# Kernel tuning notes

Hardware: AMD Instinct MI355X
Metric: run time of the kernel (lower is better)

Reference implementation:

```python
import jax, jax.numpy as jnp
import numpy as np

B, C, H, W = 4, 256, 64, 64
G = 32          # GroupNorm groups
EPS = 1e-6


def setup_inputs() -> dict:
    key = jax.random.key(0)
    ks = jax.random.split(key, 6)
    inp = {
        "x": jax.random.normal(ks[0], (B, C, H, W), dtype=jnp.float32),
        "gamma": jnp.ones((C,), jnp.float32),
        "beta": jnp.zeros((C,), jnp.float32),
        "wq": jax.random.normal(ks[1], (C, C), jnp.float32) * 0.02,
        "bq": jnp.zeros((C,), jnp.float32),
        "wk": jax.random.normal(ks[2], (C, C), jnp.float32) * 0.02,
        "bk": jnp.zeros((C,), jnp.float32),
        "wv": jax.random.normal(ks[3], (C, C), jnp.float32) * 0.02,
        "bv": jnp.zeros((C,), jnp.float32),
        "wp": jax.random.normal(ks[4], (C, C), jnp.float32) * 0.02,
        "bp": jnp.zeros((C,), jnp.float32),
    }
    return inp


def _group_norm(x, gamma, beta):
    b, c, h, w = x.shape
    xs = x.reshape(b, G, c // G, h, w)
    mu = xs.mean(axis=(2, 3, 4), keepdims=True)
    var = xs.var(axis=(2, 3, 4), keepdims=True)  # biased, matches torch GroupNorm
    xn = ((xs - mu) * jax.lax.rsqrt(var + EPS)).reshape(b, c, h, w)
    return xn * gamma[None, :, None, None] + beta[None, :, None, None]


def _conv1x1(s, w, bias):
    # 1x1 conv == per-pixel channel matmul
    return jnp.einsum('oc,bchw->bohw', w, s) + bias[None, :, None, None]


def reference(x, gamma, beta, wq, bq, wk, bk, wv, bv, wp, bp):
    b, c, h, w = x.shape
    s = _group_norm(x, gamma, beta)
    q = _conv1x1(s, wq, bq).reshape(b, c, h * w)  # [B, C, N]
    k = _conv1x1(s, wk, bk).reshape(b, c, h * w)
    v = _conv1x1(s, wv, bv).reshape(b, c, h * w)
    # scores[b,i,j] = sum_c q[b,c,i] k[b,c,j], scaled by C^-1/2
    scores = jnp.einsum('bci,bcj->bij', q, k) * (c ** -0.5)
    attn = jax.nn.softmax(scores, axis=2)
    # h_[b,c,i] = sum_j v[b,c,j] attn[b,i,j]
    h_ = jnp.einsum('bij,bcj->bci', attn, v).reshape(b, c, h, w)
    h_ = _conv1x1(h_, wp, bp)
    return x + h_
```

## Files before the change

### kernel.cpp

```cpp
#include <hip/hip_runtime.h>

#define BB 4
#define CCH 256
#define NPIX 4096
#define EPS 1e-6f

typedef __attribute__((ext_vector_type(8))) short bf16x8;
typedef __attribute__((ext_vector_type(4))) float f32x4;

__device__ __forceinline__ unsigned short f2bf(float f) {
    return (unsigned short)((__float_as_uint(f) + 0x8000u) >> 16);
}
__device__ __forceinline__ float bf2f(unsigned short h) {
    return __uint_as_float((unsigned)h << 16);
}
__device__ __forceinline__ void gl2lds16(const void* g, void* l) {
    __builtin_amdgcn_global_load_lds(
        (const __attribute__((address_space(1))) unsigned int*)g,
        (__attribute__((address_space(3))) unsigned int*)l, 16, 0, 0);
}

__global__ __launch_bounds__(256) void gn_apply(const float* __restrict__ x,
                                                const float* __restrict__ gamma,
                                                const float* __restrict__ beta,
                                                unsigned short* __restrict__ sb) {
    int bg = blockIdx.x;
    int b = bg >> 5, g = bg & 31;
    const float4* x4 = (const float4*)(x + (size_t)(b * CCH + g * 8) * NPIX);
    float s = 0.f, ss = 0.f;
    for (int e = threadIdx.x; e < 8 * NPIX / 4; e += 256) {
        float4 v = x4[e];
        s += v.x + v.y + v.z + v.w;
        ss += v.x * v.x + v.y * v.y + v.z * v.z + v.w * v.w;
    }
    __shared__ float rs[256], rss[256];
    __shared__ float mean_s, rstd_s;
    rs[threadIdx.x] = s; rss[threadIdx.x] = ss;
    __syncthreads();
    for (int off = 128; off > 0; off >>= 1) {
        if (threadIdx.x < (unsigned)off) {
            rs[threadIdx.x] += rs[threadIdx.x + off];
            rss[threadIdx.x] += rss[threadIdx.x + off];
        }
        __syncthreads();
    }
    if (threadIdx.x == 0) {
        const float inv = 1.0f / (float)(8 * NPIX);
        float m = rs[0] * inv;
        float var = rss[0] * inv - m * m;
        mean_s = m;
        rstd_s = rsqrtf(var + EPS);
    }
    __syncthreads();
    float scale[8], shift[8];
#pragma unroll
    for (int ci = 0; ci < 8; ++ci) {
        float ga = gamma[g * 8 + ci], be = beta[g * 8 + ci];
        scale[ci] = rstd_s * ga;
        shift[ci] = be - mean_s * scale[ci];
    }
#pragma unroll 1
    for (int r = 0; r < 4; ++r) {
        int pq = r * 256 + threadIdx.x;
        __align__(16) unsigned short h[4][8];
#pragma unroll
        for (int ci = 0; ci < 8; ++ci) {
            float4 v = x4[ci * 1024 + pq];
            h[0][ci] = f2bf(v.x * scale[ci] + shift[ci]);
            h[1][ci] = f2bf(v.y * scale[ci] + shift[ci]);
            h[2][ci] = f2bf(v.z * scale[ci] + shift[ci]);
            h[3][ci] = f2bf(v.w * scale[ci] + shift[ci]);
        }
        size_t base = ((size_t)(b * NPIX + pq * 4) << 8) + g * 8;
#pragma unroll
        for (int p = 0; p < 4; ++p)
            *(uint4*)(sb + base + (size_t)p * 256) = *(const uint4*)h[p];
    }
}

__global__ __launch_bounds__(256) void wcvt(const float* __restrict__ wq,
                                            const float* __restrict__ wk,
                                            const float* __restrict__ wv,
                                            const float* __restrict__ wp,
                                            unsigned short* __restrict__ wb) {
    int e = blockIdx.x * 256 + threadIdx.x;
    const float* srcs[4] = {wp, wq, wk, wv};
#pragma unroll
    for (int m = 0; m < 4; ++m) {
        float4 v = ((const float4*)srcs[m])[e];
        ushort4 h;
        h.x = f2bf(v.x); h.y = f2bf(v.y); h.z = f2bf(v.z); h.w = f2bf(v.w);
        *(ushort4*)(wb + (size_t)m * 65536 + (size_t)e * 4) = h;
    }
}

__global__ __launch_bounds__(256) void qkv_mfma(
    const unsigned short* __restrict__ sb, const unsigned short* __restrict__ wb,
    const float* __restrict__ bq, const float* __restrict__ bk,
    const float* __restrict__ bv,
    unsigned short* __restrict__ qT, unsigned short* __restrict__ kT,
    unsigned short* __restrict__ vB) {
    __shared__ __align__(16) char lds[34816];
    const int tid = threadIdx.x, lane = tid & 63, w = tid >> 6;
    const int ln15 = lane & 15, q = lane >> 4;
    const int n0 = blockIdx.x * 128;
    const int co0 = blockIdx.y * 128;
    const int z = blockIdx.z;
    const unsigned short* wm = wb + (size_t)(z + 1) * 65536;
    const float* bias = (z == 0) ? bq : (z == 1) ? bk : bv;

    f32x4 acc[2][8];
#pragma unroll
    for (int i2 = 0; i2 < 2; ++i2)
#pragma unroll
        for (int nf = 0; nf < 8; ++nf) {
            acc[i2][nf][0] = 0.f; acc[i2][nf][1] = 0.f;
            acc[i2][nf][2] = 0.f; acc[i2][nf][3] = 0.f;
        }

#pragma unroll 1
    for (int kt = 0; kt < 4; ++kt) {
#pragma unroll
        for (int r = 0; r < 4; ++r) {
            int gch = r * 256 + tid;
            int row = gch >> 3, sidx = gch & 7;
            int cc = sidx ^ (row & 7);
            gl2lds16(sb + ((size_t)(n0 + row) << 8) + kt * 64 + cc * 8,
                     &lds[r * 4096 + w * 1024]);
            gl2lds16(wm + ((size_t)(co0 + row) << 8) + kt * 64 + cc * 8,
                     &lds[16384 + r * 4096 + w * 1024]);
        }
        __syncthreads();
#pragma unroll
        for (int kk = 0; kk < 2; ++kk) {
            int kc = kk * 4 + q;
            bf16x8 af[2], bf[8];
#pragma unroll
            for (int i2 = 0; i2 < 2; ++i2) {
                int row = w * 32 + i2 * 16 + ln15;
                af[i2] = *(const bf16x8*)&lds[row * 128 + ((kc ^ (row & 7)) << 4)];
            }
#pragma unroll
            for (int nf = 0; nf < 8; ++nf) {
                int row = nf * 16 + ln15;
                bf[nf] = *(const bf16x8*)&lds[16384 + row * 128 + ((kc ^ (row & 7)) << 4)];
            }
#pragma unroll
            for (int i2 = 0; i2 < 2; ++i2)
#pragma unroll
                for (int nf = 0; nf < 8; ++nf)
                    acc[i2][nf] = __builtin_amdgcn_mfma_f32_16x16x32_bf16(
                        af[i2], bf[nf], acc[i2][nf], 0, 0, 0);
        }
        __syncthreads();
    }

    float bias_l[8];
#pragma unroll
    for (int nf = 0; nf < 8; ++nf) bias_l[nf] = bias[co0 + nf * 16 + ln15];
    const float scl = (z == 0) ? 0.0625f : 1.0f;
    unsigned short* T = (unsigned short*)lds;
    if (z < 2) {
#pragma unroll
        for (int i2 = 0; i2 < 2; ++i2)
#pragma unroll
            for (int nf = 0; nf < 8; ++nf)
#pragma unroll
                for (int r = 0; r < 4; ++r) {
                    int n_l = w * 32 + i2 * 16 + q * 4 + r;
                    int co_l = nf * 16 + ln15;
                    T[n_l * 136 + co_l] = f2bf((acc[i2][nf][r] + bias_l[nf]) * scl);
                }
    } else {
#pragma unroll
        for (int i2 = 0; i2 < 2; ++i2)
#pragma unroll
            for (int nf = 0; nf < 8; ++nf)
#pragma unroll
                for (int r = 0; r < 4; ++r) {
                    int n_l = w * 32 + i2 * 16 + q * 4 + r;
                    int co_l = nf * 16 + ln15;
                    T[co_l * 136 + n_l] = f2bf(acc[i2][nf][r] + bias_l[nf]);
                }
    }
    __syncthreads();
    int row = tid >> 1, half = tid & 1;
    const uint4* src = (const uint4*)&T[row * 136 + half * 64];
    uint4* dst;
    if (z < 2) {
        unsigned short* qk = (z == 0) ? qT : kT;
        dst = (uint4*)(qk + ((size_t)(n0 + row) << 8) + co0 + half * 64);
    } else {
        int b2 = n0 >> 12, pix0 = n0 & 4095;
        dst = (uint4*)(vB + ((size_t)(b2 * CCH + co0 + row) << 12) + pix0 + half * 64);
    }
#pragma unroll
    for (int u = 0; u < 8; ++u) dst[u] = src[u];
}

__global__ __launch_bounds__(512, 2) void attn_mfma(
    const unsigned short* __restrict__ qT, const unsigned short* __restrict__ kT,
    const unsigned short* __restrict__ vB,
    unsigned short* __restrict__ pO, float* __restrict__ pml) {
    __shared__ __align__(16) char lds[81920];
    const int tid = threadIdx.x, lane = tid & 63, w = tid >> 6;
    const int ln15 = lane & 15, q = lane >> 4;
    const int bx = blockIdx.x;
    const int xk = bx & 7;
    const int b = xk >> 1, jqhi = xk & 1;
    const int outer = bx >> 3;
    const int jqlo = outer & 1, itile = outer >> 1;
    const int i0 = itile * 128;
    const int jbase = (jqhi * 2 + jqlo) * 1024;
    const size_t nb = (size_t)b * NPIX;
    const int ih = w >> 1, ch = w & 1;

#pragma unroll
    for (int t = 0; t < 8; ++t) {
        int gch = (w * 8 + t) * 64 + lane;
        int row = gch >> 5, sc = gch & 31;
        int cc = sc ^ (row & 7);
        gl2lds16(qT + ((nb + i0 + row) << 8) + cc * 8, &lds[(w * 8 + t) * 1024]);
    }
    __syncthreads();
    bf16x8 qf[8];
    {
        int row = w * 16 + ln15;
#pragma unroll
        for (int kb = 0; kb < 8; ++kb)
            qf[kb] = *(const bf16x8*)&lds[row * 512 + (((kb * 4 + q) ^ (row & 7)) << 4)];
    }
    __syncthreads();

    f32x4 O[2][8];
#pragma unroll
    for (int ig = 0; ig < 2; ++ig)
#pragma unroll
        for (int ns = 0; ns < 8; ++ns) {
            O[ig][ns][0] = 0.f; O[ig][ns][1] = 0.f;
            O[ig][ns][2] = 0.f; O[ig][ns][3] = 0.f;
        }
    float l_r[4];
#pragma unroll
    for (int r = 0; r < 4; ++r) l_r[r] = 0.f;

    {
        const int j0 = jbase;
#pragma unroll
        for (int t = 0; t < 4; ++t) {
            int gch = (w * 4 + t) * 64 + lane;
            int row = gch >> 5, sc = gch & 31;
            int cc = sc ^ (row & 7);
            gl2lds16(kT + ((nb + j0 + row) << 8) + cc * 8, &lds[(w * 4 + t) * 1024]);
        }
#pragma unroll
        for (int t = 0; t < 4; ++t) {
            int gch = (w * 4 + t) * 64 + lane;
            int c = gch >> 3, sv = gch & 7;
            int jc = sv ^ (c & 7);
            gl2lds16(vB + ((size_t)(b * CCH + c) << 12) + j0 + jc * 8,
                     &lds[32768 + (w * 4 + t) * 1024]);
        }
    }

#pragma unroll 1
    for (int jt = 0; jt < 16; ++jt) {
        asm volatile("s_waitcnt vmcnt(4)" ::: "memory");
        __builtin_amdgcn_s_barrier();

        f32x4 S[4];
#pragma unroll
        for (int js = 0; js < 4; ++js) {
            S[js][0] = 0.f; S[js][1] = 0.f; S[js][2] = 0.f; S[js][3] = 0.f;
        }
        __builtin_amdgcn_s_setprio(1);
#pragma unroll
        for (int kb = 0; kb < 8; ++kb)
#pragma unroll
            for (int js = 0; js < 4; ++js) {
                int jr = js * 16 + ln15;
                bf16x8 kf = *(const bf16x8*)&lds[jr * 512 + (((kb * 4 + q) ^ (jr & 7)) << 4)];
                S[js] = __builtin_amdgcn_mfma_f32_16x16x32_bf16(qf[kb], kf, S[js], 0, 0, 0);
            }
        __builtin_amdgcn_s_setprio(0);

        asm volatile("" ::: "memory");
        __builtin_amdgcn_s_barrier();
        if (jt < 15) {
            const int j0n = jbase + (jt + 1) * 64;
#pragma unroll
            for (int t = 0; t < 4; ++t) {
                int gch = (w * 4 + t) * 64 + lane;
                int row = gch >> 5, sc = gch & 31;
                int cc = sc ^ (row & 7);
                gl2lds16(kT + ((nb + j0n + row) << 8) + cc * 8,
                         &lds[(w * 4 + t) * 1024]);
            }
        }

#pragma unroll
        for (int r = 0; r < 4; ++r) {
            float p0 = __expf(S[0][r]), p1 = __expf(S[1][r]);
            float p2 = __expf(S[2][r]), p3 = __expf(S[3][r]);
            l_r[r] += (p0 + p1) + (p2 + p3);
            int il = w * 16 + q * 4 + r;
            float pv[4] = {p0, p1, p2, p3};
#pragma unroll
            for (int js = 0; js < 4; ++js) {
                int j = js * 16 + ln15;
                *(unsigned short*)&lds[65536 + il * 128 +
                    (((j >> 3) ^ (il & 7)) << 4) + ((j & 7) << 1)] = f2bf(pv[js]);
            }
        }
        asm volatile("s_waitcnt lgkmcnt(0)" ::: "memory");
        __builtin_amdgcn_sched_barrier(0);

        if (jt < 15) {
            asm volatile("s_waitcnt vmcnt(4)" ::: "memory");
        } else {
            asm volatile("s_waitcnt vmcnt(0)" ::: "memory");
        }
        __builtin_amdgcn_s_barrier();

        bf16x8 pf[2][2];
#pragma unroll
        for (int ig = 0; ig < 2; ++ig)
#pragma unroll
            for (int kf2 = 0; kf2 < 2; ++kf2) {
                int rr = ih * 32 + ig * 16 + ln15;
                pf[ig][kf2] = *(const bf16x8*)&lds[65536 + rr * 128 +
                                                  (((kf2 * 4 + q) ^ (rr & 7)) << 4)];
            }

        __builtin_amdgcn_s_setprio(1);
#pragma unroll
        for (int ns = 0; ns < 8; ++ns) {
            int c = ch * 128 + ns * 16 + ln15;
            bf16x8 vf0 = *(const bf16x8*)&lds[32768 + c * 128 + ((q ^ (c & 7)) << 4)];
            bf16x8 vf1 = *(const bf16x8*)&lds[32768 + c * 128 + (((4 + q) ^ (c & 7)) << 4)];
            O[0][ns] = __builtin_amdgcn_mfma_f32_16x16x32_bf16(pf[0][0], vf0, O[0][ns], 0, 0, 0);
            O[0][ns] = __builtin_amdgcn_mfma_f32_16x16x32_bf16(pf[0][1], vf1, O[0][ns], 0, 0, 0);
            O[1][ns] = __builtin_amdgcn_mfma_f32_16x16x32_bf16(pf[1][0], vf0, O[1][ns], 0, 0, 0);
            O[1][ns] = __builtin_amdgcn_mfma_f32_16x16x32_bf16(pf[1][1], vf1, O[1][ns], 0, 0, 0);
        }
        __builtin_amdgcn_s_setprio(0);

        asm volatile("" ::: "memory");
        __builtin_amdgcn_s_barrier();
        if (jt < 15) {
            const int j0n = jbase + (jt + 1) * 64;
#pragma unroll
            for (int t = 0; t < 4; ++t) {
                int gch = (w * 4 + t) * 64 + lane;
                int c = gch >> 3, sv = gch & 7;
                int jc = sv ^ (c & 7);
                gl2lds16(vB + ((size_t)(b * CCH + c) << 12) + j0n + jc * 8,
                         &lds[32768 + (w * 4 + t) * 1024]);
            }
        }
    }

    size_t pbase = (size_t)bx * (128 * 256);
#pragma unroll
    for (int ig = 0; ig < 2; ++ig)
#pragma unroll
        for (int ns = 0; ns < 8; ++ns) {
            int c = ch * 128 + ns * 16 + ln15;
#pragma unroll
            for (int r = 0; r < 4; ++r) {
                int i = ih * 32 + ig * 16 + q * 4 + r;
                pO[pbase + i * 256 + c] = f2bf(O[ig][ns][r]);
            }
        }
#pragma unroll
    for (int r = 0; r < 4; ++r) {
        float l = l_r[r];
        l += __shfl_xor(l, 1);
        l += __shfl_xor(l, 2);
        l += __shfl_xor(l, 4);
        l += __shfl_xor(l, 8);
        if (ln15 == 0) {
            int i = w * 16 + q * 4 + r;
            pml[bx * 128 + i] = l;
        }
    }
}

__global__ __launch_bounds__(256) void attn_merge(
    const unsigned short* __restrict__ pO, const float* __restrict__ pml,
    unsigned short* __restrict__ hN) {
    int bid = blockIdx.x;
    int b = bid & 3, itile = (bid >> 2) & 31, ih = (bid >> 7) & 1;
    int base = itile * 16 + b * 2;
    const int offs[4] = {0, 1, 8, 9};
    __shared__ float fs[64];
    int t = threadIdx.x;
    if (t < 64) {
        float l = 0.f;
#pragma unroll
        for (int s = 0; s < 4; ++s)
            l += pml[(base + offs[s]) * 128 + ih * 64 + t];
        fs[t] = 1.0f / l;
    }
    __syncthreads();
    int i = t >> 2, cq = t & 3;
    float f = fs[i];
    int row = ih * 64 + i;
    size_t nrow = ((size_t)(b * NPIX + itile * 128 + row)) << 8;
#pragma unroll
    for (int p = 0; p < 16; ++p) {
        int c = p * 16 + cq * 4;
        float o0 = 0.f, o1 = 0.f, o2 = 0.f, o3 = 0.f;
#pragma unroll
        for (int s = 0; s < 4; ++s) {
            ushort4 a = *(const ushort4*)&pO[(size_t)(base + offs[s]) * 32768 + row * 256 + c];
            o0 += bf2f(a.x); o1 += bf2f(a.y); o2 += bf2f(a.z); o3 += bf2f(a.w);
        }
        ushort4 h;
        h.x = f2bf(o0 * f); h.y = f2bf(o1 * f);
        h.z = f2bf(o2 * f); h.w = f2bf(o3 * f);
        *(ushort4*)&hN[nrow + c] = h;
    }
}

__global__ __launch_bounds__(256) void proj_mfma(
    const unsigned short* __restrict__ hN, const unsigned short* __restrict__ wb,
    const float* __restrict__ bp, const float* __restrict__ x,
    float* __restrict__ out) {
    __shared__ __align__(16) char lds[34816];
    const int tid = threadIdx.x, lane = tid & 63, w = tid >> 6;
    const int ln15 = lane & 15, q = lane >> 4;
    const int n0 = blockIdx.x * 128;
    const int co0 = blockIdx.y * 128;

    f32x4 acc[2][8];
#pragma unroll
    for (int i2 = 0; i2 < 2; ++i2)
#pragma unroll
        for (int nf = 0; nf < 8; ++nf) {
            acc[i2][nf][0] = 0.f; acc[i2][nf][1] = 0.f;
            acc[i2][nf][2] = 0.f; acc[i2][nf][3] = 0.f;
        }

#pragma unroll 1
    for (int kt = 0; kt < 4; ++kt) {
#pragma unroll
        for (int r = 0; r < 4; ++r) {
            int gch = r * 256 + tid;
            int row = gch >> 3, sidx = gch & 7;
            int cc = sidx ^ (row & 7);
            gl2lds16(hN + ((size_t)(n0 + row) << 8) + kt * 64 + cc * 8,
                     &lds[r * 4096 + w * 1024]);
            gl2lds16(wb + ((size_t)(co0 + row) << 8) + kt * 64 + cc * 8,
                     &lds[16384 + r * 4096 + w * 1024]);
        }
        __syncthreads();
#pragma unroll
        for (int kk = 0; kk < 2; ++kk) {
            int kc = kk * 4 + q;
            bf16x8 af[2], bf[8];
#pragma unroll
            for (int i2 = 0; i2 < 2; ++i2) {
                int row = w * 32 + i2 * 16 + ln15;
                af[i2] = *(const bf16x8*)&lds[row * 128 + ((kc ^ (row & 7)) << 4)];
            }
#pragma unroll
            for (int nf = 0; nf < 8; ++nf) {
                int row = nf * 16 + ln15;
                bf[nf] = *(const bf16x8*)&lds[16384 + row * 128 + ((kc ^ (row & 7)) << 4)];
            }
#pragma unroll
            for (int i2 = 0; i2 < 2; ++i2)
#pragma unroll
                for (int nf = 0; nf < 8; ++nf)
                    acc[i2][nf] = __builtin_amdgcn_mfma_f32_16x16x32_bf16(
                        af[i2], bf[nf], acc[i2][nf], 0, 0, 0);
        }
        __syncthreads();
    }

    unsigned short* T = (unsigned short*)lds;
#pragma unroll
    for (int i2 = 0; i2 < 2; ++i2)
#pragma unroll
        for (int nf = 0; nf < 8; ++nf)
#pragma unroll
            for (int r = 0; r < 4; ++r) {
                int n_l = w * 32 + i2 * 16 + q * 4 + r;
                int co_l = nf * 16 + ln15;
                T[co_l * 136 + n_l] = f2bf(acc[i2][nf][r]);
            }
    __syncthreads();
    int row = tid >> 1, half = tid & 1;
    int b2 = n0 >> 12, pix0 = n0 & 4095;
    float br = bp[co0 + row];
    size_t gidx = (((size_t)(b2 * CCH + co0 + row)) << 12) + pix0 + half * 64;
    const unsigned short* trow = &T[row * 136 + half * 64];
#pragma unroll
    for (int u = 0; u < 16; ++u) {
        float4 xv = *(const float4*)&x[gidx + u * 4];
        ushort4 tv = *(const ushort4*)&trow[u * 4];
        float4 o;
        o.x = xv.x + br + bf2f(tv.x);
        o.y = xv.y + br + bf2f(tv.y);
        o.z = xv.z + br + bf2f(tv.z);
        o.w = xv.w + br + bf2f(tv.w);
        *(float4*)&out[gidx + u * 4] = o;
    }
}

extern "C" void kernel_launch(void* const* d_in, const int* in_sizes, int n_in,
                              void* d_out, int out_size, void* d_ws, size_t ws_size,
                              hipStream_t stream) {
    const float* x     = (const float*)d_in[0];
    const float* gamma = (const float*)d_in[1];
    const float* beta  = (const float*)d_in[2];
    const float* wq    = (const float*)d_in[3];
    const float* bq    = (const float*)d_in[4];
    const float* wk    = (const float*)d_in[5];
    const float* bk    = (const float*)d_in[6];
    const float* wv    = (const float*)d_in[7];
    const float* bv    = (const float*)d_in[8];
    const float* wp    = (const float*)d_in[9];
    const float* bp    = (const float*)d_in[10];
    float* out = (float*)d_out;

    char* p = (char*)d_ws;
    unsigned short* sb  = (unsigned short*)p; p += 8388608;
    unsigned short* hN  = sb;
    unsigned short* wb  = (unsigned short*)p; p += 524288;
    unsigned short* pO  = (unsigned short*)p; p += 33554432;
    float*          pml = (float*)p;          p += 262144;
    unsigned short* qT  = (unsigned short*)p; p += 8388608;
    unsigned short* kT  = (unsigned short*)p; p += 8388608;
    unsigned short* vB  = (unsigned short*)p;

    gn_apply<<<BB * 32, 256, 0, stream>>>(x, gamma, beta, sb);
    wcvt<<<64, 256, 0, stream>>>(wq, wk, wv, wp, wb);
    qkv_mfma<<<dim3(128, 2, 3), 256, 0, stream>>>(sb, wb, bq, bk, bv, qT, kT, vB);
    attn_mfma<<<512, 512, 0, stream>>>(qT, kT, vB, pO, pml);
    attn_merge<<<256, 256, 0, stream>>>(pO, pml, hN);
    proj_mfma<<<dim3(128, 2), 256, 0, stream>>>(hN, wb, bp, x, out);
}
```

Baseline: 240.3 us.

## Switch attention MFMAs to 32x32x16 tiles and repartition waves over i/j/c

The attention kernel moves from 16x16x32 to 32x32x16 bf16 MFMA instructions for both QK^T and PV. For QK^T, each wave now owns a 32x32 score tile (four i-groups times two j-halves), with the channel dimension split over two accumulators that are summed before exp. For PV, each wave owns a 64x64 block of (i, c). Row sums are now produced per j-half, so the partial-sum buffer doubles and the merge kernel adds both halves. The larger MFMA tiles are meant to cut LDS fragment reads and instruction count per flop, at the cost of bigger accumulators and a different LDS access pattern for P writes.

```diff
diff --git a/kernel.cpp b/kernel.cpp
--- a/kernel.cpp
+++ b/kernel.cpp
@@ -7,6 +7,7 @@
 
 typedef __attribute__((ext_vector_type(8))) short bf16x8;
 typedef __attribute__((ext_vector_type(4))) float f32x4;
+typedef __attribute__((ext_vector_type(16))) float f32x16;
 
 __device__ __forceinline__ unsigned short f2bf(float f) {
     return (unsigned short)((__float_as_uint(f) + 0x8000u) >> 16);
@@ -204,7 +205,7 @@
     unsigned short* __restrict__ pO, float* __restrict__ pml) {
     __shared__ __align__(16) char lds[81920];
     const int tid = threadIdx.x, lane = tid & 63, w = tid >> 6;
-    const int ln15 = lane & 15, q = lane >> 4;
+    const int l31 = lane & 31, lh = lane >> 5;
     const int bx = blockIdx.x;
     const int xk = bx & 7;
     const int b = xk >> 1, jqhi = xk & 1;
@@ -213,7 +214,10 @@
     const int i0 = itile * 128;
     const int jbase = (jqhi * 2 + jqlo) * 1024;
     const size_t nb = (size_t)b * NPIX;
-    const int ih = w >> 1, ch = w & 1;
+    const int iqb = (w >> 1) * 32;
+    const int jh = w & 1, jwb = jh * 32;
+    const int ipb = (w & 1) * 64;
+    const int cqb = (w >> 1) * 64;
 
 #pragma unroll
     for (int t = 0; t < 8; ++t) {
@@ -223,26 +227,27 @@
         gl2lds16(qT + ((nb + i0 + row) << 8) + cc * 8, &lds[(w * 8 + t) * 1024]);
     }
     __syncthreads();
-    bf16x8 qf[8];
+    bf16x8 qf[16];
     {
-        int row = w * 16 + ln15;
-#pragma unroll
-        for (int kb = 0; kb < 8; ++kb)
-            qf[kb] = *(const bf16x8*)&lds[row * 512 + (((kb * 4 + q) ^ (row & 7)) << 4)];
-    }
-    __syncthreads();
-
-    f32x4 O[2][8];
+        int row = iqb + l31;
+#pragma unroll
+        for (int kc = 0; kc < 16; ++kc) {
+            int sc = kc * 2 + lh;
+            qf[kc] = *(const bf16x8*)&lds[row * 512 + ((sc ^ (row & 7)) << 4)];
+        }
+    }
+    __syncthreads();
+
+    f32x16 O[2][2];
 #pragma unroll
     for (int ig = 0; ig < 2; ++ig)
 #pragma unroll
-        for (int ns = 0; ns < 8; ++ns) {
-            O[ig][ns][0] = 0.f; O[ig][ns][1] = 0.f;
-            O[ig][ns][2] = 0.f; O[ig][ns][3] = 0.f;
-        }
-    float l_r[4];
-#pragma unroll
-    for (int r = 0; r < 4; ++r) l_r[r] = 0.f;
+        for (int cg = 0; cg < 2; ++cg)
+#pragma unroll
+            for (int r = 0; r < 16; ++r) O[ig][cg][r] = 0.f;
+    float l_acc[16];
+#pragma unroll
+    for (int r = 0; r < 16; ++r) l_acc[r] = 0.f;
 
     {
         const int j0 = jbase;
@@ -268,20 +273,23 @@
         asm volatile("s_waitcnt vmcnt(4)" ::: "memory");
         __builtin_amdgcn_s_barrier();
 
-        f32x4 S[4];
-#pragma unroll
-        for (int js = 0; js < 4; ++js) {
-            S[js][0] = 0.f; S[js][1] = 0.f; S[js][2] = 0.f; S[js][3] = 0.f;
-        }
+        f32x16 S0, S1;
+#pragma unroll
+        for (int r = 0; r < 16; ++r) { S0[r] = 0.f; S1[r] = 0.f; }
         __builtin_amdgcn_s_setprio(1);
-#pragma unroll
-        for (int kb = 0; kb < 8; ++kb)
-#pragma unroll
-            for (int js = 0; js < 4; ++js) {
-                int jr = js * 16 + ln15;
-                bf16x8 kf = *(const bf16x8*)&lds[jr * 512 + (((kb * 4 + q) ^ (jr & 7)) << 4)];
-                S[js] = __builtin_amdgcn_mfma_f32_16x16x32_bf16(qf[kb], kf, S[js], 0, 0, 0);
-            }
+        {
+            int krow = jwb + l31;
+            int ksw = krow * 512;
+#pragma unroll
+            for (int kc = 0; kc < 8; ++kc) {
+                int sc0 = (2 * kc) * 2 + lh;
+                int sc1 = (2 * kc + 1) * 2 + lh;
+                bf16x8 k0 = *(const bf16x8*)&lds[ksw + ((sc0 ^ (krow & 7)) << 4)];
+                bf16x8 k1 = *(const bf16x8*)&lds[ksw + ((sc1 ^ (krow & 7)) << 4)];
+                S0 = __builtin_amdgcn_mfma_f32_32x32x16_bf16(qf[2 * kc], k0, S0, 0, 0, 0);
+                S1 = __builtin_amdgcn_mfma_f32_32x32x16_bf16(qf[2 * kc + 1], k1, S1, 0, 0, 0);
+            }
+        }
         __builtin_amdgcn_s_setprio(0);
 
         asm volatile("" ::: "memory");
@@ -298,18 +306,17 @@
             }
         }
 
-#pragma unroll
-        for (int r = 0; r < 4; ++r) {
-            float p0 = __expf(S[0][r]), p1 = __expf(S[1][r]);
-            float p2 = __expf(S[2][r]), p3 = __expf(S[3][r]);
-            l_r[r] += (p0 + p1) + (p2 + p3);
-            int il = w * 16 + q * 4 + r;
-            float pv[4] = {p0, p1, p2, p3};
-#pragma unroll
-            for (int js = 0; js < 4; ++js) {
-                int j = js * 16 + ln15;
-                *(unsigned short*)&lds[65536 + il * 128 +
-                    (((j >> 3) ^ (il & 7)) << 4) + ((j & 7) << 1)] = f2bf(pv[js]);
+        {
+            int col = jwb + l31;
+            int chs = (col >> 3) << 4;
+            int cof = (col & 7) << 1;
+#pragma unroll
+            for (int r = 0; r < 16; ++r) {
+                float p = __expf(S0[r] + S1[r]);
+                l_acc[r] += p;
+                int row = iqb + (r & 3) + 8 * (r >> 2) + 4 * lh;
+                *(unsigned short*)&lds[65536 + row * 128 +
+                    (chs ^ ((row & 7) << 4)) + cof] = f2bf(p);
             }
         }
         asm volatile("s_waitcnt lgkmcnt(0)" ::: "memory");
@@ -322,26 +329,22 @@
         }
         __builtin_amdgcn_s_barrier();
 
-        bf16x8 pf[2][2];
-#pragma unroll
-        for (int ig = 0; ig < 2; ++ig)
-#pragma unroll
-            for (int kf2 = 0; kf2 < 2; ++kf2) {
-                int rr = ih * 32 + ig * 16 + ln15;
-                pf[ig][kf2] = *(const bf16x8*)&lds[65536 + rr * 128 +
-                                                  (((kf2 * 4 + q) ^ (rr & 7)) << 4)];
-            }
-
         __builtin_amdgcn_s_setprio(1);
-#pragma unroll
-        for (int ns = 0; ns < 8; ++ns) {
-            int c = ch * 128 + ns * 16 + ln15;
-            bf16x8 vf0 = *(const bf16x8*)&lds[32768 + c * 128 + ((q ^ (c & 7)) << 4)];
-            bf16x8 vf1 = *(const bf16x8*)&lds[32768 + c * 128 + (((4 + q) ^ (c & 7)) << 4)];
-            O[0][ns] = __builtin_amdgcn_mfma_f32_16x16x32_bf16(pf[0][0], vf0, O[0][ns], 0, 0, 0);
-            O[0][ns] = __builtin_amdgcn_mfma_f32_16x16x32_bf16(pf[0][1], vf1, O[0][ns], 0, 0, 0);
-            O[1][ns] = __builtin_amdgcn_mfma_f32_16x16x32_bf16(pf[1][0], vf0, O[1][ns], 0, 0, 0);
-            O[1][ns] = __builtin_amdgcn_mfma_f32_16x16x32_bf16(pf[1][1], vf1, O[1][ns], 0, 0, 0);
+        {
+            int pr0 = ipb + l31, pr1 = ipb + 32 + l31;
+            int vc0 = cqb + l31, vc1 = cqb + 32 + l31;
+#pragma unroll
+            for (int kc = 0; kc < 4; ++kc) {
+                int pc = kc * 2 + lh;
+                bf16x8 pf0 = *(const bf16x8*)&lds[65536 + pr0 * 128 + ((pc ^ (pr0 & 7)) << 4)];
+                bf16x8 pf1 = *(const bf16x8*)&lds[65536 + pr1 * 128 + ((pc ^ (pr1 & 7)) << 4)];
+                bf16x8 vf0 = *(const bf16x8*)&lds[32768 + vc0 * 128 + ((pc ^ (vc0 & 7)) << 4)];
+                bf16x8 vf1 = *(const bf16x8*)&lds[32768 + vc1 * 128 + ((pc ^ (vc1 & 7)) << 4)];
+                O[0][0] = __builtin_amdgcn_mfma_f32_32x32x16_bf16(pf0, vf0, O[0][0], 0, 0, 0);
+                O[0][1] = __builtin_amdgcn_mfma_f32_32x32x16_bf16(pf0, vf1, O[0][1], 0, 0, 0);
+                O[1][0] = __builtin_amdgcn_mfma_f32_32x32x16_bf16(pf1, vf0, O[1][0], 0, 0, 0);
+                O[1][1] = __builtin_amdgcn_mfma_f32_32x32x16_bf16(pf1, vf1, O[1][1], 0, 0, 0);
+            }
         }
         __builtin_amdgcn_s_setprio(0);
 
@@ -364,24 +367,24 @@
 #pragma unroll
     for (int ig = 0; ig < 2; ++ig)
 #pragma unroll
-        for (int ns = 0; ns < 8; ++ns) {
-            int c = ch * 128 + ns * 16 + ln15;
-#pragma unroll
-            for (int r = 0; r < 4; ++r) {
-                int i = ih * 32 + ig * 16 + q * 4 + r;
-                pO[pbase + i * 256 + c] = f2bf(O[ig][ns][r]);
-            }
-        }
-#pragma unroll
-    for (int r = 0; r < 4; ++r) {
-        float l = l_r[r];
+        for (int cg = 0; cg < 2; ++cg)
+#pragma unroll
+            for (int r = 0; r < 16; ++r) {
+                int i = ipb + ig * 32 + (r & 3) + 8 * (r >> 2) + 4 * lh;
+                int c = cqb + cg * 32 + l31;
+                pO[pbase + i * 256 + c] = f2bf(O[ig][cg][r]);
+            }
+#pragma unroll
+    for (int r = 0; r < 16; ++r) {
+        float l = l_acc[r];
         l += __shfl_xor(l, 1);
         l += __shfl_xor(l, 2);
         l += __shfl_xor(l, 4);
         l += __shfl_xor(l, 8);
-        if (ln15 == 0) {
-            int i = w * 16 + q * 4 + r;
-            pml[bx * 128 + i] = l;
+        l += __shfl_xor(l, 16);
+        if (l31 == 0) {
+            int row = iqb + (r & 3) + 8 * (r >> 2) + 4 * lh;
+            pml[bx * 256 + jh * 128 + row] = l;
         }
     }
 }
@@ -398,8 +401,10 @@
     if (t < 64) {
         float l = 0.f;
 #pragma unroll
-        for (int s = 0; s < 4; ++s)
-            l += pml[(base + offs[s]) * 128 + ih * 64 + t];
+        for (int s = 0; s < 4; ++s) {
+            int px = (base + offs[s]) * 256 + ih * 64 + t;
+            l += pml[px] + pml[px + 128];
+        }
         fs[t] = 1.0f / l;
     }
     __syncthreads();
@@ -530,7 +535,7 @@
     unsigned short* hN  = sb;
     unsigned short* wb  = (unsigned short*)p; p += 524288;
     unsigned short* pO  = (unsigned short*)p; p += 33554432;
-    float*          pml = (float*)p;          p += 262144;
+    float*          pml = (float*)p;          p += 524288;
     unsigned short* qT  = (unsigned short*)p; p += 8388608;
     unsigned short* kT  = (unsigned short*)p; p += 8388608;
     unsigned short* vB  = (unsigned short*)p;
```

After: 236.6 us. Within noise of the previous version (-1.5%).
